# Kernel optimization log

Measured on AMD Instinct MI355X. Metric: run time of the kernel, lower is better.

## Reference

```python
import jax, jax.numpy as jnp
import numpy as np

NEG_INF = -jnp.inf


def _rope(x, cos, sin):
    # x: (B, S, H, D); cos/sin: (1, S, 1, D//2)
    xr = x.reshape(*x.shape[:-1], -1, 2)
    x1, x2 = xr[..., 0], xr[..., 1]  # (B, S, H, D//2) each
    # faithful to source: concat halves along last axis, same total size D
    return jnp.concatenate([x1 * cos - x2 * sin, x1 * sin + x2 * cos], axis=-1)


def setup_inputs() -> dict:
    B, S, D, H, Ld = 2, 2048, 2048, 16, 128
    key = jax.random.key(0)
    ks = jax.random.split(key, 6)
    sc = 1.0 / np.sqrt(D)
    return {
        "x": jax.random.normal(ks[0], (B, S, D), jnp.float32),
        "attn_mask": jnp.ones((B, S), jnp.int32),
        "Wq": jax.random.normal(ks[1], (D, H * Ld), jnp.float32) * sc,
        "bq": jnp.zeros((H * Ld,), jnp.float32),
        "Wk": jax.random.normal(ks[2], (D, H * Ld), jnp.float32) * sc,
        "bk": jnp.zeros((H * Ld,), jnp.float32),
        "Wv": jax.random.normal(ks[3], (D, H * Ld), jnp.float32) * sc,
        "bv": jnp.zeros((H * Ld,), jnp.float32),
        "Wo": jax.random.normal(ks[4], (H * Ld, D), jnp.float32) * sc,
        "bo": jnp.zeros((D,), jnp.float32),
        "num_heads": H,
    }


def reference(x, attn_mask, Wq, bq, Wk, bk, Wv, bv, Wo, bo, num_heads):
    B, S, D = x.shape
    H = int(num_heads)
    Ld = Wq.shape[1] // H
    base = 10000

    q = (x @ Wq + bq).reshape(B, S, H, Ld)
    k = (x @ Wk + bk).reshape(B, S, H, Ld)
    v = (x @ Wv + bv).reshape(B, S, H, Ld)

    # rotary tables (match RotaryEmbedding.setup, sliced to seq_len)
    inv_freq = 1.0 / base ** (2 * jnp.arange(0, Ld // 2) / Ld)
    angles = jnp.arange(S)[:, None] * inv_freq[None, :]  # (S, Ld//2)
    cos = jnp.cos(angles)[None, :, None, :].astype(x.dtype)
    sin = jnp.sin(angles)[None, :, None, :].astype(x.dtype)
    q = _rope(q, cos, sin)
    k = _rope(k, cos, sin)

    q = jnp.transpose(q, (0, 2, 1, 3))  # (B, H, S, Ld)
    k = jnp.transpose(k, (0, 2, 1, 3))
    v = jnp.transpose(v, (0, 2, 1, 3))

    scale = jnp.sqrt(jnp.float32(Ld)).astype(x.dtype)
    scores = jnp.einsum('bnqd,bnkd->bnqk', q, k) / scale  # (B, H, S, S)

    # faithful mask from source: keep where arange[None,:] >= arange[:,None]
    row_idx = jnp.arange(S)[None, :]
    col_idx = jnp.arange(S)[:, None]
    keep = row_idx >= col_idx  # (S, S)
    scores = jnp.where(keep[None, None, :, :], scores, NEG_INF)

    # padding mask applied over the QUERY axis, as in source: (B,1,S,1)
    scores = jnp.where(attn_mask[:, None, :, None] > 0, scores, NEG_INF)

    attn = jax.nn.softmax(scores, axis=-1)
    attended = jnp.einsum('bnqk,bnkd->bnqd', attn, v)
    attended = jnp.transpose(attended, (0, 2, 1, 3)).reshape(B, S, H * Ld)
    return attended @ Wo + bo
```

## Files before the change

kernel.cpp:

```cpp
#include <hip/hip_runtime.h>
#include <math.h>

typedef __bf16 bf16x8 __attribute__((ext_vector_type(8)));
typedef float f32x4 __attribute__((ext_vector_type(4)));

#define MFMA_BF16(a,b,c) __builtin_amdgcn_mfma_f32_16x16x32_bf16((a),(b),(c),0,0,0)

static constexpr int S_LEN = 2048;
static constexpr int DM    = 2048;
static constexpr int NHEAD = 16;
static constexpr int LDH   = 128;
static constexpr int BATCH = 2;
static constexpr size_t QKV_SEG = (size_t)BATCH * NHEAD * S_LEN * LDH;

__device__ __forceinline__ unsigned short f2bf(float f) {
    unsigned u = __float_as_uint(f);
    u += 0x7fffu + ((u >> 16) & 1u);
    return (unsigned short)(u >> 16);
}
__device__ __forceinline__ float bf2f(unsigned short h) {
    return __uint_as_float(((unsigned)h) << 16);
}
__device__ __forceinline__ float fexp2(float x) { return exp2f(x); }

__device__ __forceinline__ void ld_lds16(const void* g, void* l) {
    __builtin_amdgcn_global_load_lds(
        (const __attribute__((address_space(1))) unsigned int*)g,
        (__attribute__((address_space(3))) unsigned int*)l, 16, 0, 0);
}

__global__ void convert_f32_bf16(const float* __restrict__ in,
                                 unsigned short* __restrict__ out, int n4) {
    int idx = blockIdx.x * blockDim.x + threadIdx.x;
    if (idx >= n4) return;
    float4 v = reinterpret_cast<const float4*>(in)[idx];
    unsigned lo = (unsigned)f2bf(v.x) | ((unsigned)f2bf(v.y) << 16);
    unsigned hi = (unsigned)f2bf(v.z) | ((unsigned)f2bf(v.w) << 16);
    reinterpret_cast<uint2*>(out)[idx] = make_uint2(lo, hi);
}

__global__ void gen_tab(float* __restrict__ ct, float* __restrict__ st) {
    int i = threadIdx.x & 63;
    int s = blockIdx.x * 4 + (threadIdx.x >> 6);
    float freq = (float)exp(-(double)(2 * i) / 128.0 * 9.210340371976184);
    float a = (float)s * freq;
    ct[s * 64 + i] = cosf(a);
    st[s * 64 + i] = sinf(a);
}

__global__ void wconv_t4(const float* __restrict__ W0, const float* __restrict__ W1,
                         const float* __restrict__ W2, const float* __restrict__ W3,
                         unsigned short* __restrict__ O0, unsigned short* __restrict__ O1,
                         unsigned short* __restrict__ O2, unsigned short* __restrict__ O3) {
    __shared__ unsigned short tile[32][33];
    int z = blockIdx.z;
    const float* W = (z == 0) ? W0 : (z == 1) ? W1 : (z == 2) ? W2 : W3;
    unsigned short* Wt = (z == 0) ? O0 : (z == 1) ? O1 : (z == 2) ? O2 : O3;
    int n0 = blockIdx.x * 32;
    int k0 = blockIdx.y * 32;
    int t = threadIdx.x;
    int ir = t >> 3, ic = (t & 7) * 4;
    float4 v = *reinterpret_cast<const float4*>(&W[(size_t)(k0 + ir) * DM + n0 + ic]);
    tile[ir][ic + 0] = f2bf(v.x);
    tile[ir][ic + 1] = f2bf(v.y);
    tile[ir][ic + 2] = f2bf(v.z);
    tile[ir][ic + 3] = f2bf(v.w);
    __syncthreads();
    unsigned lo = (unsigned)tile[ic + 0][ir] | ((unsigned)tile[ic + 1][ir] << 16);
    unsigned hi = (unsigned)tile[ic + 2][ir] | ((unsigned)tile[ic + 3][ir] << 16);
    *reinterpret_cast<uint2*>(&Wt[(size_t)(n0 + ir) * DM + k0 + ic]) = make_uint2(lo, hi);
}

__global__ __launch_bounds__(256, 2) void gemm_bf16_out(
    const unsigned short* __restrict__ A,
    const unsigned short* __restrict__ Bt,
    const float* __restrict__ b0,
    float* __restrict__ outp)
{
    const int K = DM;
    __shared__ __attribute__((aligned(16))) unsigned short smem[8192];
    unsigned short* As = smem;
    unsigned short* Bs = smem + 4096;
    int t = threadIdx.x;
    int m0 = blockIdx.y * 128, n0 = blockIdx.x * 128;
    int lane = t & 63, i16 = lane & 15, quad = lane >> 4;
    int w = t >> 6;
    int wm = (w >> 1) * 64, wn = (w & 1) * 64;

    f32x4 acc[4][4];
    const f32x4 z4 = {0.f, 0.f, 0.f, 0.f};
    for (int mi = 0; mi < 4; ++mi)
        for (int ni = 0; ni < 4; ++ni) acc[mi][ni] = z4;

    for (int kk = 0; kk < K; kk += 32) {
        __syncthreads();
#pragma unroll
        for (int j = 0; j < 2; ++j) {
            int off = j * 4096 + w * 1024 + lane * 16;
            int row = off >> 6;
            int g = ((off >> 4) & 3) ^ ((row >> 1) & 3);
            ld_lds16(&A [(size_t)(m0 + row) * K + kk + g * 8], (char*)As + off);
            ld_lds16(&Bt[(size_t)(n0 + row) * K + kk + g * 8], (char*)Bs + off);
        }
        __syncthreads();

        bf16x8 aF[4], bF[4];
#pragma unroll
        for (int mi = 0; mi < 4; ++mi) {
            int rA = wm + mi * 16 + i16;
            aF[mi] = *reinterpret_cast<const bf16x8*>(
                (const char*)As + rA * 64 + ((quad ^ ((rA >> 1) & 3)) * 16));
        }
#pragma unroll
        for (int ni = 0; ni < 4; ++ni) {
            int rB = wn + ni * 16 + i16;
            bF[ni] = *reinterpret_cast<const bf16x8*>(
                (const char*)Bs + rB * 64 + ((quad ^ ((rB >> 1) & 3)) * 16));
        }
#pragma unroll
        for (int mi = 0; mi < 4; ++mi)
#pragma unroll
            for (int ni = 0; ni < 4; ++ni)
                acc[mi][ni] = MFMA_BF16(aF[mi], bF[ni], acc[mi][ni]);
    }

    for (int mi = 0; mi < 4; ++mi) {
        for (int ni = 0; ni < 4; ++ni) {
            int nn = n0 + wn + ni * 16 + i16;
            float bv = b0[nn];
            for (int r = 0; r < 4; ++r) {
                int mm = m0 + wm + mi * 16 + quad * 4 + r;
                outp[(size_t)mm * DM + nn] = acc[mi][ni][r] + bv;
            }
        }
    }
}

__global__ __launch_bounds__(256, 2) void gemm_qkv_v2(
    const unsigned short* __restrict__ A,
    const unsigned short* __restrict__ Bt,
    const float* __restrict__ b0, const float* __restrict__ b1,
    const float* __restrict__ b2,
    const float* __restrict__ ctab, const float* __restrict__ stab,
    unsigned short* __restrict__ outp)
{
    constexpr int K  = DM;
    constexpr int NT = K / 32;
    constexpr int SLOT_B = 24576;
    __shared__ __attribute__((aligned(16))) unsigned short smem[36864];

    int t = threadIdx.x, lane = t & 63, w = t >> 6;
    int i16 = lane & 15, quad = lane >> 4;
    int wc = w & 1, wr = w >> 1;

    int flat = blockIdx.y * 48 + blockIdx.x;
    int xcd = flat & 7, r8 = flat >> 3;
    int nbx = xcd * 6 + (r8 >> 4);
    int nby = r8 & 15;
    int m0 = nby * 256, n0 = nbx * 128;

    const unsigned short* ga[4];
    const unsigned short* gb[2];
    int loffA[4], loffB[2];
#pragma unroll
    for (int j = 0; j < 4; ++j) {
        int off = j * 4096 + t * 16;
        int row = off >> 6;
        int g = ((off >> 4) & 3) ^ ((row >> 1) & 3);
        ga[j] = A + (size_t)(m0 + row) * K + g * 8;
        loffA[j] = off;
    }
#pragma unroll
    for (int j = 0; j < 2; ++j) {
        int off = j * 4096 + t * 16;
        int row = off >> 6;
        int g = ((off >> 4) & 3) ^ ((row >> 1) & 3);
        gb[j] = Bt + (size_t)(n0 + row) * K + g * 8;
        loffB[j] = off;
    }

    auto stage = [&](int slot, int kt) {
        char* base = (char*)smem + slot * SLOT_B;
#pragma unroll
        for (int j = 0; j < 4; ++j)
            ld_lds16(ga[j] + kt * 32, base + loffA[j]);
#pragma unroll
        for (int j = 0; j < 2; ++j)
            ld_lds16(gb[j] + kt * 32, base + 16384 + loffB[j]);
    };

    f32x4 acc[8][4];
    const f32x4 z4 = {0.f, 0.f, 0.f, 0.f};
#pragma unroll
    for (int mi = 0; mi < 8; ++mi)
#pragma unroll
        for (int ni = 0; ni < 4; ++ni) acc[mi][ni] = z4;

    auto compute = [&](int slot) {
        const char* Ab = (const char*)smem + slot * SLOT_B;
        const char* Bb = Ab + 16384;
        bf16x8 bF[4];
#pragma unroll
        for (int ni = 0; ni < 4; ++ni) {
            int rB = wc * 64 + ni * 16 + i16;
            bF[ni] = *reinterpret_cast<const bf16x8*>(
                Bb + rB * 64 + ((quad ^ ((rB >> 1) & 3)) * 16));
        }
#pragma unroll
        for (int h = 0; h < 2; ++h) {
            bf16x8 aF[4];
#pragma unroll
            for (int mi = 0; mi < 4; ++mi) {
                int rA = wr * 128 + h * 64 + mi * 16 + i16;
                aF[mi] = *reinterpret_cast<const bf16x8*>(
                    Ab + rA * 64 + ((quad ^ ((rA >> 1) & 3)) * 16));
            }
            __builtin_amdgcn_s_setprio(1);
#pragma unroll
            for (int mi = 0; mi < 4; ++mi)
#pragma unroll
                for (int ni = 0; ni < 4; ++ni)
                    acc[h * 4 + mi][ni] = MFMA_BF16(aF[mi], bF[ni], acc[h * 4 + mi][ni]);
            __builtin_amdgcn_s_setprio(0);
        }
    };

    stage(0, 0); stage(1, 1);
    asm volatile("s_waitcnt vmcnt(6)" ::: "memory");
    __builtin_amdgcn_s_barrier();
    asm volatile("" ::: "memory");

    int cs = 0, ssl = 2;
    for (int tt = 0; tt < NT - 2; ++tt) {
        stage(ssl, tt + 2);
        compute(cs);
        asm volatile("s_waitcnt vmcnt(6)" ::: "memory");
        __builtin_amdgcn_s_barrier();
        asm volatile("" ::: "memory");
        cs  = (cs  == 2) ? 0 : cs  + 1;
        ssl = (ssl == 2) ? 0 : ssl + 1;
    }
    compute(cs);
    asm volatile("s_waitcnt vmcnt(0)" ::: "memory");
    __builtin_amdgcn_s_barrier();
    asm volatile("" ::: "memory");
    cs = (cs == 2) ? 0 : cs + 1;
    compute(cs);
    __syncthreads();

    unsigned short* Cs = smem;
    int which = n0 >> 11;
    int hh = (n0 & 2047) >> 7;
    const float* bp = (which == 0) ? b0 : ((which == 1) ? b1 : b2);
    int segn = n0 & 2047;
    int bb = m0 >> 11, s0 = m0 & 2047;

    if (which == 2) {
#pragma unroll
        for (int mi = 0; mi < 8; ++mi)
#pragma unroll
            for (int ni = 0; ni < 4; ++ni) {
                int d = wc * 64 + ni * 16 + i16;
                float bv = bp[segn + d];
#pragma unroll
                for (int r = 0; r < 4; ++r) {
                    int sl = wr * 128 + mi * 16 + quad * 4 + r;
                    Cs[d * 256 + (((sl >> 3) ^ (d & 31)) * 8) + (sl & 7)] =
                        f2bf(acc[mi][ni][r] + bv);
                }
            }
        __syncthreads();
        unsigned short* vout = outp + 2 * QKV_SEG;
#pragma unroll
        for (int it = 0; it < 16; ++it) {
            int idx = it * 256 + t;
            int d = idx >> 5, sg = idx & 31;
            uint4 v = *reinterpret_cast<const uint4*>(
                &Cs[d * 256 + ((sg ^ (d & 31)) * 8)]);
            size_t oidx = (((size_t)(bb * NHEAD + hh)) * LDH + d) * S_LEN + s0 + sg * 8;
            *reinterpret_cast<uint4*>(vout + oidx) = v;
        }
    } else {
#pragma unroll
        for (int mi = 0; mi < 8; ++mi)
#pragma unroll
            for (int ni = 0; ni < 4; ++ni) {
                int nl = wc * 64 + ni * 16 + i16;
                float bv = bp[segn + nl];
#pragma unroll
                for (int r = 0; r < 4; ++r) {
                    int ml = wr * 128 + mi * 16 + quad * 4 + r;
                    Cs[ml * 128 + nl] = f2bf(acc[mi][ni][r] + bv);
                }
            }
        __syncthreads();
        float qscale = (which == 0) ? (0.08838834764831845f * 1.4426950408889634f) : 1.0f;
        unsigned short* qout = outp + (size_t)which * QKV_SEG;
#pragma unroll
        for (int it = 0; it < 16; ++it) {
            int idx = it * 256 + t;
            int row = idx >> 4, c16 = idx & 15;
            int mm = m0 + row;
            int ss = mm & 2047, bb2 = mm >> 11;
            int i8 = (c16 & 7) * 8;
            const unsigned short* crow = Cs + row * 128 + i8 * 2;
            uint4 w0 = *reinterpret_cast<const uint4*>(crow);
            uint4 w1 = *reinterpret_cast<const uint4*>(crow + 8);
            unsigned pw[8] = {w0.x, w0.y, w0.z, w0.w, w1.x, w1.y, w1.z, w1.w};
            float4 cA = *reinterpret_cast<const float4*>(&ctab[ss * 64 + i8]);
            float4 cB = *reinterpret_cast<const float4*>(&ctab[ss * 64 + i8 + 4]);
            float4 sA = *reinterpret_cast<const float4*>(&stab[ss * 64 + i8]);
            float4 sB = *reinterpret_cast<const float4*>(&stab[ss * 64 + i8 + 4]);
            float cv[8] = {cA.x, cA.y, cA.z, cA.w, cB.x, cB.y, cB.z, cB.w};
            float sv[8] = {sA.x, sA.y, sA.z, sA.w, sB.x, sB.y, sB.z, sB.w};
            bool hi = (c16 >= 8);
            unsigned short ov[8];
#pragma unroll
            for (int j = 0; j < 8; ++j) {
                float xe = bf2f((unsigned short)(pw[j] & 0xffff));
                float xo = bf2f((unsigned short)(pw[j] >> 16));
                float o = hi ? (xe * sv[j] + xo * cv[j]) : (xe * cv[j] - xo * sv[j]);
                ov[j] = f2bf(o * qscale);
            }
            size_t oidx = (((size_t)(bb2 * NHEAD + hh)) * S_LEN + ss) * LDH + c16 * 8;
            *reinterpret_cast<uint4*>(qout + oidx) =
                *reinterpret_cast<const uint4*>(ov);
        }
    }
}

__global__ __launch_bounds__(256, 2) void attn_kernel(
    const unsigned short* __restrict__ q,
    const unsigned short* __restrict__ k,
    const unsigned short* __restrict__ vt,
    unsigned short* __restrict__ att)
{
    __shared__ __attribute__((aligned(16))) unsigned short Ks[2][64 * 128];
    __shared__ __attribute__((aligned(16))) unsigned short Vs[2][128 * 64];
    __shared__ __attribute__((aligned(16))) unsigned short Ps[4][32 * 64];

    int bid = blockIdx.x;
    int second = bid >> 8;
    int p = bid & 255;
    int xb = second ? (15 - (p >> 5)) : (p >> 5);
    int bh = p & 31;
    int b = bh >> 4, h = bh & (NHEAD - 1);
    int q0 = xb * 128;

    int t = threadIdx.x, w = t >> 6, lane = t & 63;
    int i16 = lane & 15, quad = lane >> 4;
    int qbase = q0 + w * 32;

    bf16x8 qf[2][4];
#pragma unroll
    for (int qs = 0; qs < 2; ++qs) {
        const unsigned short* qrow = q + ((size_t)bh * S_LEN + qbase + qs * 16 + i16) * LDH;
#pragma unroll
        for (int c = 0; c < 4; ++c)
            qf[qs][c] = *reinterpret_cast<const bf16x8*>(qrow + c * 32 + quad * 8);
    }

    const f32x4 z4 = {0.f, 0.f, 0.f, 0.f};
    f32x4 o[2][8];
#pragma unroll
    for (int qs = 0; qs < 2; ++qs)
#pragma unroll
        for (int dt = 0; dt < 8; ++dt) o[qs][dt] = z4;
    float l_i[2] = {0.f, 0.f};

    const unsigned short* kbh  = k  + (size_t)bh * S_LEN * LDH;
    const unsigned short* vtbh = vt + (size_t)bh * LDH * S_LEN;
    unsigned short* PsW = Ps[w];

    auto stage = [&](int buf, int kk0) {
#pragma unroll
        for (int j = 0; j < 4; ++j) {
            int off = j * 4096 + w * 1024 + lane * 16;
            int key = off >> 8;
            int gk = ((off >> 4) & 15) ^ (key & 15);
            ld_lds16(&kbh[(size_t)(kk0 + key) * LDH + gk * 8], (char*)Ks[buf] + off);
            int d = off >> 7;
            int gv = ((off >> 4) & 7) ^ (d & 7);
            ld_lds16(&vtbh[(size_t)d * S_LEN + kk0 + gv * 8], (char*)Vs[buf] + off);
        }
    };

    stage(0, q0);
    int nch = (S_LEN - q0) >> 6;
    for (int ci = 0; ci < nch; ++ci) {
        __syncthreads();
        if (ci + 1 < nch) stage((ci + 1) & 1, q0 + (ci + 1) * 64);
        int kk0 = q0 + ci * 64;
        if (kk0 + 64 <= qbase) continue;
        const unsigned short* Kb = Ks[ci & 1];
        const unsigned short* Vb = Vs[ci & 1];

        f32x4 s[2][4];
#pragma unroll
        for (int qs = 0; qs < 2; ++qs)
#pragma unroll
            for (int kn = 0; kn < 4; ++kn) s[qs][kn] = z4;
#pragma unroll
        for (int c = 0; c < 4; ++c) {
            bf16x8 kf[4];
#pragma unroll
            for (int kn = 0; kn < 4; ++kn) {
                int key = kn * 16 + i16;
                int gs = (c * 4 + quad) ^ (key & 15);
                kf[kn] = *reinterpret_cast<const bf16x8*>((const char*)Kb + key * 256 + gs * 16);
            }
#pragma unroll
            for (int qs = 0; qs < 2; ++qs)
#pragma unroll
                for (int kn = 0; kn < 4; ++kn)
                    s[qs][kn] = MFMA_BF16(kf[kn], qf[qs][c], s[qs][kn]);
        }

        bool diag = (kk0 < qbase + 32);
#pragma unroll
        for (int qs = 0; qs < 2; ++qs) {
            int q_local = qs * 16 + i16;
            int qg = qbase + q_local;
#pragma unroll
            for (int kn = 0; kn < 4; ++kn) {
                int keyb = kk0 + kn * 16 + quad * 4;
                float pv[4];
                if (diag) {
#pragma unroll
                    for (int r = 0; r < 4; ++r)
                        pv[r] = (keyb + r >= qg) ? fexp2(s[qs][kn][r]) : 0.f;
                } else {
#pragma unroll
                    for (int r = 0; r < 4; ++r) pv[r] = fexp2(s[qs][kn][r]);
                }
                l_i[qs] += (pv[0] + pv[1]) + (pv[2] + pv[3]);
                unsigned lo = (unsigned)f2bf(pv[0]) | ((unsigned)f2bf(pv[1]) << 16);
                unsigned hi = (unsigned)f2bf(pv[2]) | ((unsigned)f2bf(pv[3]) << 16);
                int g = (kn * 2 + (quad >> 1)) ^ (q_local & 7);
                char* addr = (char*)PsW + q_local * 128 + g * 16 + (quad & 1) * 8;
                *reinterpret_cast<uint2*>(addr) = make_uint2(lo, hi);
            }
        }

#pragma unroll
        for (int hh = 0; hh < 2; ++hh) {
            bf16x8 pf[2];
#pragma unroll
            for (int qs = 0; qs < 2; ++qs) {
                int q_local = qs * 16 + i16;
                int g = (hh * 4 + quad) ^ (q_local & 7);
                pf[qs] = *reinterpret_cast<const bf16x8*>((const char*)PsW + q_local * 128 + g * 16);
            }
#pragma unroll
            for (int dt = 0; dt < 8; ++dt) {
                int d = dt * 16 + i16;
                int gv = (hh * 4 + quad) ^ (d & 7);
                bf16x8 vf = *reinterpret_cast<const bf16x8*>((const char*)Vb + d * 128 + gv * 16);
                o[0][dt] = MFMA_BF16(pf[0], vf, o[0][dt]);
                o[1][dt] = MFMA_BF16(pf[1], vf, o[1][dt]);
            }
        }
    }

#pragma unroll
    for (int qs = 0; qs < 2; ++qs) {
        float lr = l_i[qs];
        lr += __shfl_xor(lr, 16);
        lr += __shfl_xor(lr, 32);
        l_i[qs] = lr;
    }
#pragma unroll
    for (int qs = 0; qs < 2; ++qs) {
#pragma unroll
        for (int r = 0; r < 4; ++r) {
            float lv = __shfl(l_i[qs], quad * 4 + r);
            float inv = 1.0f / lv;
            int qrow = qbase + qs * 16 + quad * 4 + r;
            unsigned short* orow = att + ((size_t)b * S_LEN + qrow) * DM + h * LDH;
#pragma unroll
            for (int dt = 0; dt < 8; ++dt)
                orow[dt * 16 + i16] = f2bf(o[qs][dt][r] * inv);
        }
    }
}

extern "C" void kernel_launch(void* const* d_in, const int* in_sizes, int n_in,
                              void* d_out, int out_size, void* d_ws, size_t ws_size,
                              hipStream_t stream) {
    const float* x  = (const float*)d_in[0];
    const float* Wq = (const float*)d_in[2];
    const float* bq = (const float*)d_in[3];
    const float* Wk = (const float*)d_in[4];
    const float* bk = (const float*)d_in[5];
    const float* Wv = (const float*)d_in[6];
    const float* bv = (const float*)d_in[7];
    const float* Wo = (const float*)d_in[8];
    const float* bo = (const float*)d_in[9];

    char* ws = (char*)d_ws;
    unsigned short* xb  = (unsigned short*)(ws);
    unsigned short* Wqt = (unsigned short*)(ws + 16777216);
    unsigned short* Wkt = (unsigned short*)(ws + 25165824);
    unsigned short* Wvt = (unsigned short*)(ws + 33554432);
    unsigned short* Wot = (unsigned short*)(ws + 41943040);
    unsigned short* qkv = (unsigned short*)(ws + 50331648);
    unsigned short* att = (unsigned short*)(ws + 100663296);
    float* ctab = (float*)(ws + 117440512);
    float* stab = (float*)(ws + 117964800);

    convert_f32_bf16<<<8192, 256, 0, stream>>>(x, xb, (BATCH * S_LEN * DM) / 4);
    gen_tab<<<512, 256, 0, stream>>>(ctab, stab);
    wconv_t4<<<dim3(64, 64, 4), 256, 0, stream>>>(Wq, Wk, Wv, Wo, Wqt, Wkt, Wvt, Wot);

    gemm_qkv_v2<<<dim3(48, 16), 256, 0, stream>>>(
        xb, Wqt, bq, bk, bv, ctab, stab, qkv);

    attn_kernel<<<512, 256, 0, stream>>>(qkv, qkv + QKV_SEG, qkv + 2 * QKV_SEG, att);

    gemm_bf16_out<<<dim3(DM / 128, (BATCH * S_LEN) / 128), 256, 0, stream>>>(
        att, Wot, bo, (float*)d_out);
}
```

Before: 396.0 us.

## Fuse prep kernels, pipeline output GEMM with 3-stage LDS, add MFMA priority hints

Merges the three preprocessing kernels (x conversion, rope table generation, weight transpose-conversion) into one launch dispatched by block index range. Replaces the output projection GEMM with a 256x128-tile, triple-buffered global-to-LDS pipeline that uses explicit vmcnt waits, a single barrier per step and XCD-aware block remapping. Adds s_setprio around MFMA bursts in both the output GEMM and the attention kernel. This aims to cut launch overhead and hide load latency in the output GEMM, at the cost of more LDS and registers and a grid of only 256 blocks.

```diff
diff --git a/kernel.cpp b/kernel.cpp
--- a/kernel.cpp
+++ b/kernel.cpp
@@ -29,111 +29,170 @@
         (__attribute__((address_space(3))) unsigned int*)l, 16, 0, 0);
 }
 
-__global__ void convert_f32_bf16(const float* __restrict__ in,
-                                 unsigned short* __restrict__ out, int n4) {
-    int idx = blockIdx.x * blockDim.x + threadIdx.x;
-    if (idx >= n4) return;
-    float4 v = reinterpret_cast<const float4*>(in)[idx];
-    unsigned lo = (unsigned)f2bf(v.x) | ((unsigned)f2bf(v.y) << 16);
-    unsigned hi = (unsigned)f2bf(v.z) | ((unsigned)f2bf(v.w) << 16);
-    reinterpret_cast<uint2*>(out)[idx] = make_uint2(lo, hi);
-}
-
-__global__ void gen_tab(float* __restrict__ ct, float* __restrict__ st) {
-    int i = threadIdx.x & 63;
-    int s = blockIdx.x * 4 + (threadIdx.x >> 6);
-    float freq = (float)exp(-(double)(2 * i) / 128.0 * 9.210340371976184);
-    float a = (float)s * freq;
-    ct[s * 64 + i] = cosf(a);
-    st[s * 64 + i] = sinf(a);
-}
-
-__global__ void wconv_t4(const float* __restrict__ W0, const float* __restrict__ W1,
+__global__ void prep_all(const float* __restrict__ x, unsigned short* __restrict__ xb,
+                         float* __restrict__ ct, float* __restrict__ st,
+                         const float* __restrict__ W0, const float* __restrict__ W1,
                          const float* __restrict__ W2, const float* __restrict__ W3,
                          unsigned short* __restrict__ O0, unsigned short* __restrict__ O1,
                          unsigned short* __restrict__ O2, unsigned short* __restrict__ O3) {
     __shared__ unsigned short tile[32][33];
-    int z = blockIdx.z;
-    const float* W = (z == 0) ? W0 : (z == 1) ? W1 : (z == 2) ? W2 : W3;
-    unsigned short* Wt = (z == 0) ? O0 : (z == 1) ? O1 : (z == 2) ? O2 : O3;
-    int n0 = blockIdx.x * 32;
-    int k0 = blockIdx.y * 32;
+    int bid = blockIdx.x;
     int t = threadIdx.x;
-    int ir = t >> 3, ic = (t & 7) * 4;
-    float4 v = *reinterpret_cast<const float4*>(&W[(size_t)(k0 + ir) * DM + n0 + ic]);
-    tile[ir][ic + 0] = f2bf(v.x);
-    tile[ir][ic + 1] = f2bf(v.y);
-    tile[ir][ic + 2] = f2bf(v.z);
-    tile[ir][ic + 3] = f2bf(v.w);
-    __syncthreads();
-    unsigned lo = (unsigned)tile[ic + 0][ir] | ((unsigned)tile[ic + 1][ir] << 16);
-    unsigned hi = (unsigned)tile[ic + 2][ir] | ((unsigned)tile[ic + 3][ir] << 16);
-    *reinterpret_cast<uint2*>(&Wt[(size_t)(n0 + ir) * DM + k0 + ic]) = make_uint2(lo, hi);
-}
-
-__global__ __launch_bounds__(256, 2) void gemm_bf16_out(
+    if (bid < 8192) {
+        int idx = bid * 256 + t;
+        float4 v = reinterpret_cast<const float4*>(x)[idx];
+        unsigned lo = (unsigned)f2bf(v.x) | ((unsigned)f2bf(v.y) << 16);
+        unsigned hi = (unsigned)f2bf(v.z) | ((unsigned)f2bf(v.w) << 16);
+        reinterpret_cast<uint2*>(xb)[idx] = make_uint2(lo, hi);
+    } else if (bid < 8704) {
+        int i = t & 63;
+        int s = (bid - 8192) * 4 + (t >> 6);
+        float freq = (float)exp(-(double)(2 * i) / 128.0 * 9.210340371976184);
+        float a = (float)s * freq;
+        ct[s * 64 + i] = cosf(a);
+        st[s * 64 + i] = sinf(a);
+    } else {
+        int wid = bid - 8704;
+        int z = wid >> 12;
+        int rem = wid & 4095;
+        int k0 = (rem >> 6) * 32;
+        int n0 = (rem & 63) * 32;
+        const float* W = (z == 0) ? W0 : (z == 1) ? W1 : (z == 2) ? W2 : W3;
+        unsigned short* Wt = (z == 0) ? O0 : (z == 1) ? O1 : (z == 2) ? O2 : O3;
+        int ir = t >> 3, ic = (t & 7) * 4;
+        float4 v = *reinterpret_cast<const float4*>(&W[(size_t)(k0 + ir) * DM + n0 + ic]);
+        tile[ir][ic + 0] = f2bf(v.x);
+        tile[ir][ic + 1] = f2bf(v.y);
+        tile[ir][ic + 2] = f2bf(v.z);
+        tile[ir][ic + 3] = f2bf(v.w);
+        __syncthreads();
+        unsigned lo = (unsigned)tile[ic + 0][ir] | ((unsigned)tile[ic + 1][ir] << 16);
+        unsigned hi = (unsigned)tile[ic + 2][ir] | ((unsigned)tile[ic + 3][ir] << 16);
+        *reinterpret_cast<uint2*>(&Wt[(size_t)(n0 + ir) * DM + k0 + ic]) = make_uint2(lo, hi);
+    }
+}
+
+__global__ __launch_bounds__(256, 2) void gemm_out_v2(
     const unsigned short* __restrict__ A,
     const unsigned short* __restrict__ Bt,
     const float* __restrict__ b0,
     float* __restrict__ outp)
 {
-    const int K = DM;
-    __shared__ __attribute__((aligned(16))) unsigned short smem[8192];
-    unsigned short* As = smem;
-    unsigned short* Bs = smem + 4096;
-    int t = threadIdx.x;
-    int m0 = blockIdx.y * 128, n0 = blockIdx.x * 128;
-    int lane = t & 63, i16 = lane & 15, quad = lane >> 4;
-    int w = t >> 6;
-    int wm = (w >> 1) * 64, wn = (w & 1) * 64;
-
-    f32x4 acc[4][4];
+    constexpr int K  = DM;
+    constexpr int NT = K / 32;
+    constexpr int SLOT_B = 24576;
+    __shared__ __attribute__((aligned(16))) unsigned short smem[36864];
+
+    int t = threadIdx.x, lane = t & 63, w = t >> 6;
+    int i16 = lane & 15, quad = lane >> 4;
+    int wc = w & 1, wr = w >> 1;
+
+    int flat = blockIdx.y * 16 + blockIdx.x;
+    int xcd = flat & 7, r8 = flat >> 3;
+    int nbx = xcd * 2 + (r8 >> 4);
+    int nby = r8 & 15;
+    int m0 = nby * 256, n0 = nbx * 128;
+
+    const unsigned short* ga[4];
+    const unsigned short* gb[2];
+    int loffA[4], loffB[2];
+#pragma unroll
+    for (int j = 0; j < 4; ++j) {
+        int off = j * 4096 + t * 16;
+        int row = off >> 6;
+        int g = ((off >> 4) & 3) ^ ((row >> 1) & 3);
+        ga[j] = A + (size_t)(m0 + row) * K + g * 8;
+        loffA[j] = off;
+    }
+#pragma unroll
+    for (int j = 0; j < 2; ++j) {
+        int off = j * 4096 + t * 16;
+        int row = off >> 6;
+        int g = ((off >> 4) & 3) ^ ((row >> 1) & 3);
+        gb[j] = Bt + (size_t)(n0 + row) * K + g * 8;
+        loffB[j] = off;
+    }
+
+    auto stage = [&](int slot, int kt) {
+        char* base = (char*)smem + slot * SLOT_B;
+#pragma unroll
+        for (int j = 0; j < 4; ++j)
+            ld_lds16(ga[j] + kt * 32, base + loffA[j]);
+#pragma unroll
+        for (int j = 0; j < 2; ++j)
+            ld_lds16(gb[j] + kt * 32, base + 16384 + loffB[j]);
+    };
+
+    f32x4 acc[8][4];
     const f32x4 z4 = {0.f, 0.f, 0.f, 0.f};
-    for (int mi = 0; mi < 4; ++mi)
+#pragma unroll
+    for (int mi = 0; mi < 8; ++mi)
+#pragma unroll
         for (int ni = 0; ni < 4; ++ni) acc[mi][ni] = z4;
 
-    for (int kk = 0; kk < K; kk += 32) {
-        __syncthreads();
-#pragma unroll
-        for (int j = 0; j < 2; ++j) {
-            int off = j * 4096 + w * 1024 + lane * 16;
-            int row = off >> 6;
-            int g = ((off >> 4) & 3) ^ ((row >> 1) & 3);
-            ld_lds16(&A [(size_t)(m0 + row) * K + kk + g * 8], (char*)As + off);
-            ld_lds16(&Bt[(size_t)(n0 + row) * K + kk + g * 8], (char*)Bs + off);
-        }
-        __syncthreads();
-
-        bf16x8 aF[4], bF[4];
-#pragma unroll
-        for (int mi = 0; mi < 4; ++mi) {
-            int rA = wm + mi * 16 + i16;
-            aF[mi] = *reinterpret_cast<const bf16x8*>(
-                (const char*)As + rA * 64 + ((quad ^ ((rA >> 1) & 3)) * 16));
-        }
+    auto compute = [&](int slot) {
+        const char* Ab = (const char*)smem + slot * SLOT_B;
+        const char* Bb = Ab + 16384;
+        bf16x8 bF[4];
 #pragma unroll
         for (int ni = 0; ni < 4; ++ni) {
-            int rB = wn + ni * 16 + i16;
+            int rB = wc * 64 + ni * 16 + i16;
             bF[ni] = *reinterpret_cast<const bf16x8*>(
-                (const char*)Bs + rB * 64 + ((quad ^ ((rB >> 1) & 3)) * 16));
-        }
-#pragma unroll
-        for (int mi = 0; mi < 4; ++mi)
-#pragma unroll
-            for (int ni = 0; ni < 4; ++ni)
-                acc[mi][ni] = MFMA_BF16(aF[mi], bF[ni], acc[mi][ni]);
-    }
-
-    for (int mi = 0; mi < 4; ++mi) {
+                Bb + rB * 64 + ((quad ^ ((rB >> 1) & 3)) * 16));
+        }
+#pragma unroll
+        for (int h = 0; h < 2; ++h) {
+            bf16x8 aF[4];
+#pragma unroll
+            for (int mi = 0; mi < 4; ++mi) {
+                int rA = wr * 128 + h * 64 + mi * 16 + i16;
+                aF[mi] = *reinterpret_cast<const bf16x8*>(
+                    Ab + rA * 64 + ((quad ^ ((rA >> 1) & 3)) * 16));
+            }
+            __builtin_amdgcn_s_setprio(1);
+#pragma unroll
+            for (int mi = 0; mi < 4; ++mi)
+#pragma unroll
+                for (int ni = 0; ni < 4; ++ni)
+                    acc[h * 4 + mi][ni] = MFMA_BF16(aF[mi], bF[ni], acc[h * 4 + mi][ni]);
+            __builtin_amdgcn_s_setprio(0);
+        }
+    };
+
+    stage(0, 0); stage(1, 1);
+    asm volatile("s_waitcnt vmcnt(6)" ::: "memory");
+    __builtin_amdgcn_s_barrier();
+    asm volatile("" ::: "memory");
+
+    int cs = 0, ssl = 2;
+    for (int tt = 0; tt < NT - 2; ++tt) {
+        stage(ssl, tt + 2);
+        compute(cs);
+        asm volatile("s_waitcnt vmcnt(6)" ::: "memory");
+        __builtin_amdgcn_s_barrier();
+        asm volatile("" ::: "memory");
+        cs  = (cs  == 2) ? 0 : cs  + 1;
+        ssl = (ssl == 2) ? 0 : ssl + 1;
+    }
+    compute(cs);
+    asm volatile("s_waitcnt vmcnt(0)" ::: "memory");
+    __builtin_amdgcn_s_barrier();
+    asm volatile("" ::: "memory");
+    cs = (cs == 2) ? 0 : cs + 1;
+    compute(cs);
+
+#pragma unroll
+    for (int mi = 0; mi < 8; ++mi)
+#pragma unroll
         for (int ni = 0; ni < 4; ++ni) {
-            int nn = n0 + wn + ni * 16 + i16;
+            int nn = n0 + wc * 64 + ni * 16 + i16;
             float bv = b0[nn];
+#pragma unroll
             for (int r = 0; r < 4; ++r) {
-                int mm = m0 + wm + mi * 16 + quad * 4 + r;
+                int mm = m0 + wr * 128 + mi * 16 + quad * 4 + r;
                 outp[(size_t)mm * DM + nn] = acc[mi][ni][r] + bv;
             }
         }
-    }
 }
 
 __global__ __launch_bounds__(256, 2) void gemm_qkv_v2(
@@ -409,11 +468,13 @@
                 int gs = (c * 4 + quad) ^ (key & 15);
                 kf[kn] = *reinterpret_cast<const bf16x8*>((const char*)Kb + key * 256 + gs * 16);
             }
+            __builtin_amdgcn_s_setprio(1);
 #pragma unroll
             for (int qs = 0; qs < 2; ++qs)
 #pragma unroll
                 for (int kn = 0; kn < 4; ++kn)
                     s[qs][kn] = MFMA_BF16(kf[kn], qf[qs][c], s[qs][kn]);
+            __builtin_amdgcn_s_setprio(0);
         }
 
         bool diag = (kk0 < qbase + 32);
@@ -451,6 +512,7 @@
                 int g = (hh * 4 + quad) ^ (q_local & 7);
                 pf[qs] = *reinterpret_cast<const bf16x8*>((const char*)PsW + q_local * 128 + g * 16);
             }
+            __builtin_amdgcn_s_setprio(1);
 #pragma unroll
             for (int dt = 0; dt < 8; ++dt) {
                 int d = dt * 16 + i16;
@@ -459,6 +521,7 @@
                 o[0][dt] = MFMA_BF16(pf[0], vf, o[0][dt]);
                 o[1][dt] = MFMA_BF16(pf[1], vf, o[1][dt]);
             }
+            __builtin_amdgcn_s_setprio(0);
         }
     }
 
@@ -508,15 +571,13 @@
     float* ctab = (float*)(ws + 117440512);
     float* stab = (float*)(ws + 117964800);
 
-    convert_f32_bf16<<<8192, 256, 0, stream>>>(x, xb, (BATCH * S_LEN * DM) / 4);
-    gen_tab<<<512, 256, 0, stream>>>(ctab, stab);
-    wconv_t4<<<dim3(64, 64, 4), 256, 0, stream>>>(Wq, Wk, Wv, Wo, Wqt, Wkt, Wvt, Wot);
+    prep_all<<<25088, 256, 0, stream>>>(x, xb, ctab, stab,
+                                        Wq, Wk, Wv, Wo, Wqt, Wkt, Wvt, Wot);
 
     gemm_qkv_v2<<<dim3(48, 16), 256, 0, stream>>>(
         xb, Wqt, bq, bk, bv, ctab, stab, qkv);
 
     attn_kernel<<<512, 256, 0, stream>>>(qkv, qkv + QKV_SEG, qkv + 2 * QKV_SEG, att);
 
-    gemm_bf16_out<<<dim3(DM / 128, (BATCH * S_LEN) / 128), 256, 0, stream>>>(
-        att, Wot, bo, (float*)d_out);
-}
+    gemm_out_v2<<<dim3(16, 16), 256, 0, stream>>>(att, Wot, bo, (float*)d_out);
+}
```

Result: faster. 383.1 us (median of 3 runs) (-3.3%).
